# Kernel tuning notes

Measured on AMD Instinct MI355X. Metric: run time of the kernel, lower is better.

## Reference

```python
import jax, jax.numpy as jnp
import numpy as np


def setup_inputs() -> dict:
    bs, L, d, h = 4, 1024, 768, 12
    ne, nm, K, P, F, R = 42, 8, 97, 128, 256, 256
    key = jax.random.key(0)
    ks = jax.random.split(key, 16)
    seq = jax.random.normal(ks[0], (bs, L, d), jnp.float32)
    att = jax.random.uniform(ks[1], (bs, h, L, L), jnp.float32)
    mention_pos = jax.random.randint(ks[2], (bs, ne, nm), 0, 1000)
    n_men = jax.random.randint(ks[3], (bs, ne), 1, nm + 1)
    men_mask = (jnp.arange(nm)[None, None, :] < n_men[..., None]).astype(jnp.float32)
    ht_pairs = jax.random.randint(ks[4], (bs, P, 2), 0, ne)
    s = 0.02
    Wattn = jax.random.normal(ks[5], (d, R)) * s
    battn = jnp.zeros((R,), jnp.float32)
    attn_net = jax.random.normal(ks[6], (K, R)) * s
    Wlin = jax.random.normal(ks[7], (d, 3)) * s
    blin = jnp.zeros((3,), jnp.float32)
    Wseg = jax.random.normal(ks[8], (3, 3, 3, F)) * s  # HWIO conv kernel (SegNet stand-in)
    bseg = jnp.zeros((F,), jnp.float32)
    Whead = jax.random.normal(ks[9], (d + F, d)) * s
    bhead = jnp.zeros((d,), jnp.float32)
    Wtail = jax.random.normal(ks[10], (d + F, d)) * s
    btail = jnp.zeros((d,), jnp.float32)
    lim = (1.0 / (2 * d)) ** 0.5
    bilinear = jax.random.uniform(ks[11], (K, d, d), minval=-lim, maxval=lim)
    bilinear_bias = jax.random.uniform(ks[12], (K,), minval=-lim, maxval=lim)
    return dict(sequence_output=seq, attention=att, men_mask=men_mask,
                mention_pos=mention_pos, ht_pairs=ht_pairs,
                Wattn=Wattn, battn=battn, attn_net=attn_net, Wlin=Wlin, blin=blin,
                Wseg=Wseg, bseg=bseg, Whead=Whead, bhead=bhead, Wtail=Wtail,
                btail=btail, bilinear=bilinear, bilinear_bias=bilinear_bias)


def _forward(sequence_output, attention, men_mask, mention_pos, ht_pairs,
             Wattn, battn, attn_net, Wlin, blin, Wseg, bseg,
             Whead, bhead, Wtail, btail, bilinear, bilinear_bias):
    bs, L, d = sequence_output.shape
    h = attention.shape[1]
    ne, nm = mention_pos.shape[1], mention_pos.shape[2]
    K = attn_net.shape[0]
    OFFSET = 1  # BERT [CLS] offset
    pos = jnp.clip(mention_pos + OFFSET, 0, L - 1)           # [bs,ne,nm]
    b_idx = jnp.arange(bs)[:, None, None]
    # ragged mention gather from sequence_output, zero-padded like the torch loops
    emb = sequence_output[b_idx, pos] * men_mask[..., None]  # [bs,ne,nm,d]
    # per-mention attention rows; attention -> [bs,L,h,L] so we gather on token dim
    A = jnp.transpose(attention, (0, 2, 1, 3))
    m_att = A[b_idx, pos] * men_mask[..., None, None]        # [bs,ne,nm,h,L]
    cnt = jnp.maximum(men_mask.sum(-1), 1.0)                 # mentions per entity
    entity_as = m_att.sum(2) / cnt[..., None, None]          # [bs,ne,h,L] mean over mentions
    # label-wise masked attention pooling over mentions
    neg = (1.0 - men_mask)[..., None] * -1e6                 # [bs,ne,nm,1]
    scores = jnp.tanh(emb @ Wattn + battn) @ attn_net.T + neg  # [bs,ne,nm,K]
    w = jax.nn.softmax(scores, axis=-2)                      # softmax over mentions
    entity_es = jnp.einsum('benk,bend->bekd', w, emb)        # [bs,ne,K,d]
    # context-based channel map (pairwise attention overlap, mean over heads)
    ht = jnp.einsum('bihl,bjhl->bijl', entity_as, entity_as) / h  # [bs,ne,ne,L]
    ht = ht / (ht.sum(-1, keepdims=True) + 1e-5)
    fmap = jnp.einsum('bijl,bld->bijd', ht, sequence_output)      # [bs,ne,ne,d]
    x = fmap @ Wlin + blin                                        # [bs,ne,ne,3]
    seg = jax.lax.conv_general_dilated(x, Wseg, (1, 1), 'SAME',
                                       dimension_numbers=('NHWC', 'HWIO', 'NHWC'))
    attn_map = jax.nn.relu(seg + bseg)                            # [bs,ne,ne,F]
    # pairwise gather (get_hts)
    hi, ti = ht_pairs[..., 0], ht_pairs[..., 1]
    bI = jnp.arange(bs)[:, None]
    F = attn_map.shape[-1]
    htss = attn_map[bI, hi, ti].reshape(-1, F)               # [N,F]
    hss = entity_es[bI, hi].reshape(-1, K, d)                # [N,K,d]
    tss = entity_es[bI, ti].reshape(-1, K, d)
    N = hss.shape[0]
    htr = jnp.broadcast_to(htss[:, None, :], (N, K, F))
    hs = jnp.tanh(jnp.concatenate([hss, htr], -1) @ Whead + bhead)
    ts = jnp.tanh(jnp.concatenate([tss, htr], -1) @ Wtail + btail)
    logits = jnp.einsum('nkd,kdp,nkp->nk', hs, bilinear, ts) + bilinear_bias
    return logits


def reference(sequence_output, attention, men_mask, mention_pos, ht_pairs,
              Wattn, battn, attn_net, Wlin, blin, Wseg, bseg,
              Whead, bhead, Wtail, btail, bilinear, bilinear_bias):
    return _forward(sequence_output, attention, men_mask, mention_pos, ht_pairs,
                    Wattn, battn, attn_net, Wlin, blin, Wseg, bseg,
                    Whead, bhead, Wtail, btail, bilinear, bilinear_bias)
```

## Files before the change

kernel.cpp:

```cpp
#include <hip/hip_runtime.h>
#include <hip/hip_bf16.h>

#define BS 4
#define LL 1024
#define DD 768
#define HH 12
#define NE 42
#define NM 8
#define KK 97
#define PPAIR 128
#define FF 256
#define RR 256
#define NPAIR (BS*PPAIR)
#define MROWS (BS*NE*KK)
#define MT 510
#define NT32 16
#define GRID_BG (8*13*16)

typedef __attribute__((ext_vector_type(8))) short short8;
typedef __attribute__((ext_vector_type(16))) float float16;

__device__ __forceinline__ float fast_tanh(float x){
  x = fminf(fmaxf(x, -15.f), 15.f);
  float e = __expf(2.f*x);
  return 1.f - 2.f/(e + 1.f);
}
__device__ __forceinline__ unsigned short f2bf(float f){
  unsigned int u = __float_as_uint(f);
  unsigned int r = (u + 0x7FFF + ((u>>16)&1)) >> 16;
  return (unsigned short)r;
}
__device__ __forceinline__ float bf2f(unsigned short u){
  return __uint_as_float(((unsigned int)u)<<16);
}
__device__ __forceinline__ void stage16(const void* g, void* l){
  __builtin_amdgcn_global_load_lds(
      (const __attribute__((address_space(1))) void*)g,
      (__attribute__((address_space(3))) void*)l, 16, 0, 0);
}

__global__ void k_emb(const float* __restrict__ seq, const int* __restrict__ mpos,
                      const float* __restrict__ mask, float* __restrict__ emb){
  int idx = blockIdx.x;
  int t = threadIdx.x;
  int b = idx / (NE*NM);
  float mk = mask[idx];
  int pos = mpos[idx] + 1;
  pos = min(max(pos, 0), LL-1);
  const float* src = seq + ((size_t)b*LL + pos)*DD;
  float* dst = emb + (size_t)idx*DD;
  for (int dd = t; dd < DD; dd += 256) dst[dd] = mk * src[dd];
}

__global__ void k_entity_as(const float* __restrict__ att, const int* __restrict__ mpos,
                            const float* __restrict__ mask, float* __restrict__ eas){
  int idx = blockIdx.x;
  int hh = idx % HH; int be = idx / HH;
  int b = be / NE;
  int t = threadIdx.x;
  float cnt = 0.f;
  for (int m=0;m<NM;m++) cnt += mask[be*NM+m];
  float inv = 1.f / fmaxf(cnt, 1.f);
  float acc[4] = {0.f,0.f,0.f,0.f};
  for (int m=0;m<NM;m++){
    float mk = mask[be*NM+m];
    if (mk != 0.f){
      int pos = min(max(mpos[be*NM+m]+1,0), LL-1);
      const float* row = att + (((size_t)b*HH + hh)*LL + pos)*LL;
      acc[0] += mk*row[t]; acc[1] += mk*row[t+256];
      acc[2] += mk*row[t+512]; acc[3] += mk*row[t+768];
    }
  }
  float* dst = eas + (size_t)idx*LL;
  dst[t]=acc[0]*inv; dst[t+256]=acc[1]*inv; dst[t+512]=acc[2]*inv; dst[t+768]=acc[3]*inv;
}

__global__ void k_score1(const float* __restrict__ emb, const float* __restrict__ Wattn,
                         const float* __restrict__ battn, float* __restrict__ tbuf){
  int idx = blockIdx.x; int t = threadIdx.x;
  __shared__ float es[DD];
  es[t]       = emb[(size_t)idx*DD + t];
  es[t+256]   = emb[(size_t)idx*DD + t + 256];
  es[t+512]   = emb[(size_t)idx*DD + t + 512];
  __syncthreads();
  float acc = battn[t];
  for (int dd=0; dd<DD; dd++) acc += es[dd]*Wattn[dd*RR + t];
  tbuf[(size_t)idx*RR + t] = fast_tanh(acc);
}

__global__ void k_scores(const float* __restrict__ tbuf, const float* __restrict__ an,
                         const float* __restrict__ mask, float* __restrict__ w){
  int be = blockIdx.x; int t = threadIdx.x;
  __shared__ float ts_[NM*RR];
  __shared__ float an_s[64*98];
  for (int i=t; i<NM*RR; i+=128) ts_[i] = tbuf[(size_t)be*NM*RR + i];
  float acc[NM];
  #pragma unroll
  for (int m=0;m<NM;m++) acc[m] = 0.f;
  for (int rc=0; rc<RR; rc+=64){
    __syncthreads();
    for (int i=t; i<KK*64; i+=128){
      int kq = i >> 6, r = i & 63;
      an_s[r*98 + kq] = an[kq*RR + rc + r];
    }
    __syncthreads();
    if (t < KK){
      for (int m=0;m<NM;m++){
        float a = 0.f;
        for (int r=0;r<64;r++) a += ts_[m*RR + rc + r]*an_s[r*98 + t];
        acc[m] += a;
      }
    }
  }
  if (t < KK){
    float s[NM];
    #pragma unroll
    for (int m=0;m<NM;m++){
      float mk = mask[be*NM+m];
      s[m] = acc[m] + (1.f - mk)*(-1e6f);
    }
    float mx = s[0];
    #pragma unroll
    for (int m=1;m<NM;m++) mx = fmaxf(mx, s[m]);
    float sum = 0.f; float e[NM];
    #pragma unroll
    for (int m=0;m<NM;m++){ e[m] = __expf(s[m]-mx); sum += e[m]; }
    float invs = 1.f/sum;
    #pragma unroll
    for (int m=0;m<NM;m++) w[((size_t)be*NM+m)*KK + t] = e[m]*invs;
  }
}

__global__ void k_entity_es(const float* __restrict__ emb, const float* __restrict__ w,
                            unsigned short* __restrict__ esf){
  int be = blockIdx.x; int t = threadIdx.x;
  __shared__ float es[NM*DD];
  __shared__ float ws_[NM*KK];
  for (int i = t; i < NM*DD; i += 256) es[i] = emb[(size_t)be*NM*DD + i];
  for (int i = t; i < NM*KK; i += 256) ws_[i] = w[(size_t)be*NM*KK + i];
  __syncthreads();
  for (int idx = t; idx < KK*96; idx += 256){
    int k = idx % KK, d8 = idx / KK;
    int d0 = d8*8;
    float a[8] = {0,0,0,0,0,0,0,0};
    #pragma unroll
    for (int m=0;m<NM;m++){
      float wv = ws_[m*KK + k];
      #pragma unroll
      for (int j=0;j<8;j++) a[j] += wv*es[m*DD + d0 + j];
    }
    int row = be*KK + k;
    int mt = row >> 5, lr = row & 31, ds = d8 >> 1, qq = d8 & 1;
    short8 v;
    #pragma unroll
    for (int j=0;j<8;j++) v[j] = (short)f2bf(a[j]);
    *(short8*)(esf + ((((size_t)mt*48) + ds)*64 + lr + 32*qq)*8) = v;
  }
}

__global__ void k_seqlin(const float* __restrict__ seq, const float* __restrict__ Wlin,
                         float* __restrict__ sl){
  int bl = blockIdx.x; int t = threadIdx.x;
  const float* row = seq + (size_t)bl*DD;
  float a[3] = {0.f,0.f,0.f};
  for (int dd=t; dd<DD; dd+=256){
    float v = row[dd];
    a[0] += v*Wlin[dd*3+0]; a[1] += v*Wlin[dd*3+1]; a[2] += v*Wlin[dd*3+2];
  }
  __shared__ float red[256];
  float res[3];
  for (int c=0;c<3;c++){
    red[t] = a[c]; __syncthreads();
    for (int off=128; off>0; off>>=1){ if (t<off) red[t]+=red[t+off]; __syncthreads(); }
    res[c] = red[0]; __syncthreads();
  }
  if (t==0){ sl[bl*3+0]=res[0]; sl[bl*3+1]=res[1]; sl[bl*3+2]=res[2]; }
}

__global__ void k_ht_x(const float* __restrict__ eas, const float* __restrict__ sl,
                       const float* __restrict__ blin, float* __restrict__ x){
  int idx = blockIdx.x;
  int j = idx % NE; int i = (idx/NE)%NE; int b = idx/(NE*NE);
  int t = threadIdx.x;
  int w = t >> 6, lane = t & 63;
  const float* ai = eas + ((size_t)(b*NE+i))*HH*LL;
  const float* aj = eas + ((size_t)(b*NE+j))*HH*LL;
  float v[4];
  #pragma unroll
  for (int it=0; it<4; it++){
    int l = t + it*256;
    float acc=0.f;
    #pragma unroll
    for (int hh2=0; hh2<HH; hh2++) acc += ai[hh2*LL + l]*aj[hh2*LL + l];
    v[it] = acc * (1.f/HH);
  }
  __shared__ float wsum[4];
  __shared__ float xred[4][3];
  float s = v[0]+v[1]+v[2]+v[3];
  s += __shfl_xor(s, 1);  s += __shfl_xor(s, 2);  s += __shfl_xor(s, 4);
  s += __shfl_xor(s, 8);  s += __shfl_xor(s, 16); s += __shfl_xor(s, 32);
  if (lane == 0) wsum[w] = s;
  __syncthreads();
  float inv = 1.f/((wsum[0]+wsum[1]+wsum[2]+wsum[3]) + 1e-5f);
  float xa[3]={0.f,0.f,0.f};
  #pragma unroll
  for (int it=0; it<4; it++){
    int l = t + it*256;
    float wv = v[it]*inv;
    const float* s3 = sl + ((size_t)b*LL + l)*3;
    xa[0]+=wv*s3[0]; xa[1]+=wv*s3[1]; xa[2]+=wv*s3[2];
  }
  #pragma unroll
  for (int c=0;c<3;c++){
    float q = xa[c];
    q += __shfl_xor(q, 1);  q += __shfl_xor(q, 2);  q += __shfl_xor(q, 4);
    q += __shfl_xor(q, 8);  q += __shfl_xor(q, 16); q += __shfl_xor(q, 32);
    if (lane == 0) xred[w][c] = q;
  }
  __syncthreads();
  if (t < 3) x[(size_t)idx*3 + t] = xred[0][t]+xred[1][t]+xred[2][t]+xred[3][t] + blin[t];
}

__global__ void k_conv_pairs(const float* __restrict__ x, const int* __restrict__ pairs,
                             const float* __restrict__ Wseg, const float* __restrict__ bseg,
                             float* __restrict__ htss){
  int n = blockIdx.x; int t = threadIdx.x;
  int b = n / PPAIR;
  int hi = pairs[n*2+0], ti = pairs[n*2+1];
  __shared__ float xs[27];
  if (t < 27){
    int di = t/9, dj = (t/3)%3, ci = t%3;
    int ii = hi + di - 1, jj = ti + dj - 1;
    float v = 0.f;
    if (ii>=0 && ii<NE && jj>=0 && jj<NE) v = x[(((size_t)b*NE+ii)*NE+jj)*3 + ci];
    xs[t] = v;
  }
  __syncthreads();
  float acc = bseg[t];
  #pragma unroll
  for (int tap=0; tap<27; tap++) acc += xs[tap]*Wseg[tap*FF + t];
  htss[(size_t)n*FF + t] = fmaxf(acc, 0.f);
}

__global__ void k_pair_proj(const float* __restrict__ htss, const float* __restrict__ Wb,
                            const float* __restrict__ bias, float* __restrict__ outp){
  int n = blockIdx.x; int t = threadIdx.x;
  __shared__ float hs_s[FF];
  hs_s[t] = htss[(size_t)n*FF + t];
  __syncthreads();
  float a0 = bias[t], a1 = bias[t+256], a2 = bias[t+512];
  for (int r=0;r<FF;r++){
    float hv = hs_s[r];
    const float* wr = Wb + (size_t)r*DD;
    a0 += hv*wr[t]; a1 += hv*wr[t+256]; a2 += hv*wr[t+512];
  }
  float* dst = outp + (size_t)n*DD;
  dst[t]=a0; dst[t+256]=a1; dst[t+512]=a2;
}

__global__ void k_wshuffle(const float* __restrict__ src, unsigned short* __restrict__ dst){
  int bi = blockIdx.x;
  int mat = bi / 144; int r = bi % 144;
  int ds = r / 3, ntg = r % 3;
  int t = threadIdx.x;
  size_t mo = (size_t)mat*589824;
  __shared__ float ls[16][260];
  #pragma unroll
  for (int i=0;i<16;i++)
    ls[i][t] = src[mo + ((size_t)(ds*16+i))*768 + ntg*256 + t];
  __syncthreads();
  #pragma unroll
  for (int it=0; it<2; it++){
    int idx = it*256 + t;
    int pt_l = idx >> 6, lane = idx & 63;
    int nl = pt_l*32 + (lane & 31);
    int qq = lane >> 5;
    short8 v;
    #pragma unroll
    for (int j=0;j<8;j++) v[j] = (short)f2bf(ls[qq*8 + j][nl]);
    *(short8*)(dst + mo + (((size_t)ds*24 + ntg*8 + pt_l)*64 + lane)*8) = v;
  }
}

__global__ __launch_bounds__(256) void k_gemm_frag2(const unsigned short* __restrict__ Af,
    const unsigned short* __restrict__ Bh, const unsigned short* __restrict__ Bt,
    unsigned short* __restrict__ Ch, unsigned short* __restrict__ Ct){
  int mt = blockIdx.x / 6, ntg = blockIdx.x % 6;
  int t = threadIdx.x; int w = t >> 6; int lane = t & 63;
  int nt = ntg*4 + w;
  float16 acch = (float16)(0.0f), acct = (float16)(0.0f);
  const unsigned short* ap = Af + (((size_t)mt*48)*64 + lane)*8;
  const unsigned short* bph = Bh + (((size_t)nt)*64 + lane)*8;
  const unsigned short* bpt = Bt + (((size_t)nt)*64 + lane)*8;
  #pragma unroll 4
  for (int ds=0; ds<48; ds++){
    short8 a  = *(const short8*)(ap + (size_t)ds*512);
    short8 bh = *(const short8*)(bph + (size_t)ds*24*512);
    short8 bt = *(const short8*)(bpt + (size_t)ds*24*512);
    acch = __builtin_amdgcn_mfma_f32_32x32x16_bf16(a, bh, acch, 0, 0, 0);
    acct = __builtin_amdgcn_mfma_f32_32x32x16_bf16(a, bt, acct, 0, 0, 0);
  }
  int col = nt*32 + (lane & 31);
  int aq = lane >> 5;
  #pragma unroll
  for (int rI=0;rI<16;rI++){
    int row = mt*32 + (rI&3) + 8*(rI>>2) + 4*aq;
    Ch[(size_t)row*768 + col] = f2bf(acch[rI]);
    Ct[(size_t)row*768 + col] = f2bf(acct[rI]);
  }
}

__global__ void k_hsts(const unsigned short* __restrict__ Ehb, const float* __restrict__ ph,
                       const int* __restrict__ pairs, unsigned short* __restrict__ hsF){
  int bi = blockIdx.x; int nt = bi / KK; int k = bi - nt*KK;
  int t = threadIdx.x;
  __shared__ int ehB[32];
  if (t < 32){
    int n = nt*32 + t; int b = n >> 7;
    ehB[t] = ((b*NE + pairs[n*2+0])*KK + k)*DD;
  }
  __syncthreads();
  unsigned short* dst = hsF + (((size_t)nt*KK + k)*48)*512;
  #pragma unroll 2
  for (int c=0; c<12; c++){
    int L = c*256 + t;
    int ds = L >> 6, lane = L & 63;
    int r = lane & 31, q = lane >> 5;
    int n = nt*32 + r;
    int d0 = ds*16 + q*8;
    short8 ev = *(const short8*)(Ehb + ehB[r] + d0);
    float4 p0 = *(const float4*)(ph + (size_t)n*DD + d0);
    float4 p1 = *(const float4*)(ph + (size_t)n*DD + d0 + 4);
    float pf[8] = {p0.x,p0.y,p0.z,p0.w,p1.x,p1.y,p1.z,p1.w};
    short8 v;
    #pragma unroll
    for (int j=0;j<8;j++) v[j] = (short)f2bf(fast_tanh(bf2f((unsigned short)ev[j]) + pf[j]));
    *(short8*)(dst + (size_t)ds*512 + lane*8) = v;
  }
}

__global__ void k_outinit(const float* __restrict__ bias, float* __restrict__ out){
  int i = blockIdx.x*256 + threadIdx.x;
  if (i < NPAIR*KK) out[i] = bias[i % KK];
}

__global__ __launch_bounds__(512,4) void k_bil_gemm(
    const unsigned short* __restrict__ hsF, const unsigned short* __restrict__ Etb,
    const float* __restrict__ pt_, const unsigned short* __restrict__ Bfrag,
    const int* __restrict__ pairs, float* __restrict__ out){
  int xcd = blockIdx.x & 7; int g = blockIdx.x >> 3;
  int ps = g & 3; int nt = (g >> 2) & 3; int kgrp = g >> 4;
  int k = kgrp*8 + xcd;
  if (k >= KK) return;
  int n0 = nt*128;
  int t = threadIdx.x; int w = t >> 6; int lane = t & 63;
  int wr = w >> 1, wc = w & 1;
  __shared__ int etB[128];
  __shared__ unsigned short aS[2][4][512];
  __shared__ unsigned short bS[2][6][512];
  __shared__ float redbuf[4][2][32];
  if (t < 128){
    int n = n0 + t; int b = n >> 7;
    etB[t] = ((b*NE + pairs[n*2+1])*KK + k)*DD;
  }
  __syncthreads();
  int aq = lane >> 5;
  const unsigned short* gp0;
  unsigned short* lp0s[2];
  const unsigned short* gp1 = nullptr;
  unsigned short* lp1s[2] = {nullptr, nullptr};
  size_t gstep0, gstep1 = 0;
  if (w < 4){
    gp0 = hsF + (((size_t)(nt*4 + w)*KK + k)*48)*512 + lane*8;
    gstep0 = 512;
    lp0s[0] = &aS[0][w][0]; lp0s[1] = &aS[1][w][0];
  } else {
    gp0 = Bfrag + ((size_t)k*1152 + (size_t)(ps*6 + (w-4)))*512 + lane*8;
    gstep0 = 24*512;
    lp0s[0] = &bS[0][w-4][0]; lp0s[1] = &bS[1][w-4][0];
  }
  int nch = 1;
  if (w < 2){
    gp1 = Bfrag + ((size_t)k*1152 + (size_t)(ps*6 + 4 + w))*512 + lane*8;
    gstep1 = 24*512;
    lp1s[0] = &bS[0][4+w][0]; lp1s[1] = &bS[1][4+w][0];
    nch = 2;
  }
  float16 acc0 = (float16)(0.f), acc1 = (float16)(0.f), acc2 = (float16)(0.f);
  stage16(gp0, lp0s[0]);
  if (nch == 2) stage16(gp1, lp1s[0]);
  for (int ds=0; ds<48; ds++){
    int buf = ds & 1;
    if (ds < 47){
      stage16(gp0 + (size_t)(ds+1)*gstep0, lp0s[buf^1]);
      if (nch == 2) stage16(gp1 + (size_t)(ds+1)*gstep1, lp1s[buf^1]);
      if (nch == 2) asm volatile("s_waitcnt vmcnt(2)" ::: "memory");
      else          asm volatile("s_waitcnt vmcnt(1)" ::: "memory");
    } else {
      asm volatile("s_waitcnt vmcnt(0)" ::: "memory");
    }
    asm volatile("s_barrier" ::: "memory");
    short8 a  = *(const short8*)&aS[buf][wr][lane*8];
    short8 b0 = *(const short8*)&bS[buf][wc  ][lane*8];
    short8 b1 = *(const short8*)&bS[buf][wc+2][lane*8];
    short8 b2 = *(const short8*)&bS[buf][wc+4][lane*8];
    acc0 = __builtin_amdgcn_mfma_f32_32x32x16_bf16(a, b0, acc0, 0, 0, 0);
    acc1 = __builtin_amdgcn_mfma_f32_32x32x16_bf16(a, b1, acc1, 0, 0, 0);
    acc2 = __builtin_amdgcn_mfma_f32_32x32x16_bf16(a, b2, acc2, 0, 0, 0);
    asm volatile("s_barrier" ::: "memory");
  }
  int pb0 = ps*6 + wc;
  #pragma unroll
  for (int rI=0; rI<16; rI++){
    int row = (rI&3) + 8*(rI>>2) + 4*aq;
    int nloc = wr*32 + row;
    int eb = etB[nloc];
    const float* ptp = pt_ + (size_t)(n0 + nloc)*DD;
    int colb = lane & 31;
    int c0 = (pb0+0)*32 + colb, c1 = (pb0+2)*32 + colb, c2 = (pb0+4)*32 + colb;
    float s = acc0[rI]*fast_tanh(bf2f(Etb[eb + c0]) + ptp[c0])
            + acc1[rI]*fast_tanh(bf2f(Etb[eb + c1]) + ptp[c1])
            + acc2[rI]*fast_tanh(bf2f(Etb[eb + c2]) + ptp[c2]);
    s += __shfl_xor(s, 1);  s += __shfl_xor(s, 2);
    s += __shfl_xor(s, 4);  s += __shfl_xor(s, 8);
    s += __shfl_xor(s, 16);
    if ((lane & 31) == 0) redbuf[wr][wc][row] = s;
  }
  __syncthreads();
  if (t < 128){
    atomicAdd(&out[(size_t)(n0 + t)*KK + k],
              redbuf[t>>5][0][t&31] + redbuf[t>>5][1][t&31]);
  }
}

extern "C" void kernel_launch(void* const* d_in, const int* in_sizes, int n_in,
                              void* d_out, int out_size, void* d_ws, size_t ws_size,
                              hipStream_t stream){
  const float* seq      = (const float*)d_in[0];
  const float* att      = (const float*)d_in[1];
  const float* mask     = (const float*)d_in[2];
  const int*   mpos     = (const int*)d_in[3];
  const int*   pairs    = (const int*)d_in[4];
  const float* Wattn    = (const float*)d_in[5];
  const float* battn    = (const float*)d_in[6];
  const float* attn_net = (const float*)d_in[7];
  const float* Wlin     = (const float*)d_in[8];
  const float* blin     = (const float*)d_in[9];
  const float* Wseg     = (const float*)d_in[10];
  const float* bseg     = (const float*)d_in[11];
  const float* Whead    = (const float*)d_in[12];
  const float* bhead    = (const float*)d_in[13];
  const float* Wtail    = (const float*)d_in[14];
  const float* btail    = (const float*)d_in[15];
  const float* bil      = (const float*)d_in[16];
  const float* bilb     = (const float*)d_in[17];
  float* out = (float*)d_out;

  char* ws = (char*)d_ws;
  size_t off = 0;
  auto allocB = [&](size_t nbytes)->char*{
    char* p = ws + off;
    off += (nbytes + 255) & ~(size_t)255;
    return p;
  };
  unsigned short* BF     = (unsigned short*)allocB((size_t)KK*589824*2);
  unsigned short* Ehb    = (unsigned short*)allocB((size_t)MT*32*768*2);
  unsigned short* Etb    = (unsigned short*)allocB((size_t)MT*32*768*2);
  unsigned short* WheadF = (unsigned short*)allocB((size_t)589824*2);
  unsigned short* WtailF = (unsigned short*)allocB((size_t)589824*2);
  float* phb  = (float*)allocB((size_t)NPAIR*DD*4);
  float* ptb  = (float*)allocB((size_t)NPAIR*DD*4);
  size_t hsF_bytes = (size_t)NT32*KK*48*512*2;
  char* uni = allocB(hsF_bytes);
  size_t uoff = 0;
  auto ualloc = [&](size_t nbytes)->char*{
    char* p = uni + uoff;
    uoff += (nbytes + 255) & ~(size_t)255;
    return p;
  };
  float* emb  = (float*)ualloc((size_t)BS*NE*NM*DD*4);
  float* tbuf = (float*)ualloc((size_t)BS*NE*NM*RR*4);
  float* wsm  = (float*)ualloc((size_t)BS*NE*NM*KK*4);
  float* eas  = (float*)ualloc((size_t)BS*NE*HH*LL*4);
  float* sl   = (float*)ualloc((size_t)BS*LL*3*4);
  float* xb   = (float*)ualloc((size_t)BS*NE*NE*3*4);
  float* htss = (float*)ualloc((size_t)NPAIR*FF*4);
  unsigned short* esf = (unsigned short*)ualloc((size_t)MT*48*64*8*2);
  unsigned short* hsF = (unsigned short*)uni;

  k_outinit<<<(NPAIR*KK+255)/256, 256, 0, stream>>>(bilb, out);
  k_emb<<<BS*NE*NM, 256, 0, stream>>>(seq, mpos, mask, emb);
  k_score1<<<BS*NE*NM, 256, 0, stream>>>(emb, Wattn, battn, tbuf);
  k_scores<<<BS*NE, 128, 0, stream>>>(tbuf, attn_net, mask, wsm);
  k_entity_as<<<BS*NE*HH, 256, 0, stream>>>(att, mpos, mask, eas);
  k_entity_es<<<BS*NE, 256, 0, stream>>>(emb, wsm, esf);
  k_seqlin<<<BS*LL, 256, 0, stream>>>(seq, Wlin, sl);
  k_ht_x<<<BS*NE*NE, 256, 0, stream>>>(eas, sl, blin, xb);
  k_conv_pairs<<<NPAIR, 256, 0, stream>>>(xb, pairs, Wseg, bseg, htss);
  k_pair_proj<<<NPAIR, 256, 0, stream>>>(htss, Whead + 768*768, bhead, phb);
  k_pair_proj<<<NPAIR, 256, 0, stream>>>(htss, Wtail + 768*768, btail, ptb);
  k_wshuffle<<<144, 256, 0, stream>>>(Whead, WheadF);
  k_wshuffle<<<144, 256, 0, stream>>>(Wtail, WtailF);
  k_wshuffle<<<KK*144, 256, 0, stream>>>(bil, BF);
  k_gemm_frag2<<<MT*6, 256, 0, stream>>>(esf, WheadF, WtailF, Ehb, Etb);
  k_hsts<<<NT32*KK, 256, 0, stream>>>(Ehb, phb, pairs, hsF);
  k_bil_gemm<<<GRID_BG, 512, 0, stream>>>(hsF, Etb, ptb, BF, pairs, out);
}
```

Measured before the change: 892.9 us.

## Fuse small kernels and deepen bilinear GEMM K-step with unified LDS staging

Merges the mention embedding gather with the attention score projection, fuses the head and tail pair projections into a single kernel, and replaces the tree reduction in the seq-linear kernel with wavefront shuffles. The bilinear MFMA GEMM now stages two K-slices per iteration into one unified LDS buffer, halving the iteration and barrier count, and its launch-bounds occupancy hint is raised from 4 to 6. These changes aim to cut launch overhead, redundant global reads and synchronisation. The higher occupancy target may squeeze registers, and the larger LDS footprint may limit how many blocks fit per CU.

```diff
diff --git a/kernel.cpp b/kernel.cpp
--- a/kernel.cpp
+++ b/kernel.cpp
@@ -39,8 +39,10 @@
       (__attribute__((address_space(3))) void*)l, 16, 0, 0);
 }
 
-__global__ void k_emb(const float* __restrict__ seq, const int* __restrict__ mpos,
-                      const float* __restrict__ mask, float* __restrict__ emb){
+__global__ void k_emb_score1(const float* __restrict__ seq, const int* __restrict__ mpos,
+                             const float* __restrict__ mask, const float* __restrict__ Wattn,
+                             const float* __restrict__ battn, float* __restrict__ emb,
+                             float* __restrict__ tbuf){
   int idx = blockIdx.x;
   int t = threadIdx.x;
   int b = idx / (NE*NM);
@@ -49,7 +51,14 @@
   pos = min(max(pos, 0), LL-1);
   const float* src = seq + ((size_t)b*LL + pos)*DD;
   float* dst = emb + (size_t)idx*DD;
-  for (int dd = t; dd < DD; dd += 256) dst[dd] = mk * src[dd];
+  __shared__ float es[DD];
+  float v0 = mk*src[t], v1 = mk*src[t+256], v2 = mk*src[t+512];
+  es[t] = v0; es[t+256] = v1; es[t+512] = v2;
+  dst[t] = v0; dst[t+256] = v1; dst[t+512] = v2;
+  __syncthreads();
+  float acc = battn[t];
+  for (int dd=0; dd<DD; dd++) acc += es[dd]*Wattn[dd*RR + t];
+  tbuf[(size_t)idx*RR + t] = fast_tanh(acc);
 }
 
 __global__ void k_entity_as(const float* __restrict__ att, const int* __restrict__ mpos,
@@ -75,19 +84,6 @@
   dst[t]=acc[0]*inv; dst[t+256]=acc[1]*inv; dst[t+512]=acc[2]*inv; dst[t+768]=acc[3]*inv;
 }
 
-__global__ void k_score1(const float* __restrict__ emb, const float* __restrict__ Wattn,
-                         const float* __restrict__ battn, float* __restrict__ tbuf){
-  int idx = blockIdx.x; int t = threadIdx.x;
-  __shared__ float es[DD];
-  es[t]       = emb[(size_t)idx*DD + t];
-  es[t+256]   = emb[(size_t)idx*DD + t + 256];
-  es[t+512]   = emb[(size_t)idx*DD + t + 512];
-  __syncthreads();
-  float acc = battn[t];
-  for (int dd=0; dd<DD; dd++) acc += es[dd]*Wattn[dd*RR + t];
-  tbuf[(size_t)idx*RR + t] = fast_tanh(acc);
-}
-
 __global__ void k_scores(const float* __restrict__ tbuf, const float* __restrict__ an,
                          const float* __restrict__ mask, float* __restrict__ w){
   int be = blockIdx.x; int t = threadIdx.x;
@@ -161,20 +157,21 @@
 __global__ void k_seqlin(const float* __restrict__ seq, const float* __restrict__ Wlin,
                          float* __restrict__ sl){
   int bl = blockIdx.x; int t = threadIdx.x;
+  int w = t >> 6, lane = t & 63;
   const float* row = seq + (size_t)bl*DD;
-  float a[3] = {0.f,0.f,0.f};
+  float a0=0.f, a1=0.f, a2=0.f;
   for (int dd=t; dd<DD; dd+=256){
     float v = row[dd];
-    a[0] += v*Wlin[dd*3+0]; a[1] += v*Wlin[dd*3+1]; a[2] += v*Wlin[dd*3+2];
-  }
-  __shared__ float red[256];
-  float res[3];
-  for (int c=0;c<3;c++){
-    red[t] = a[c]; __syncthreads();
-    for (int off=128; off>0; off>>=1){ if (t<off) red[t]+=red[t+off]; __syncthreads(); }
-    res[c] = red[0]; __syncthreads();
-  }
-  if (t==0){ sl[bl*3+0]=res[0]; sl[bl*3+1]=res[1]; sl[bl*3+2]=res[2]; }
+    a0 += v*Wlin[dd*3+0]; a1 += v*Wlin[dd*3+1]; a2 += v*Wlin[dd*3+2];
+  }
+  #pragma unroll
+  for (int off=1; off<64; off<<=1){
+    a0 += __shfl_xor(a0, off); a1 += __shfl_xor(a1, off); a2 += __shfl_xor(a2, off);
+  }
+  __shared__ float red[4][3];
+  if (lane == 0){ red[w][0]=a0; red[w][1]=a1; red[w][2]=a2; }
+  __syncthreads();
+  if (t < 3) sl[bl*3+t] = red[0][t]+red[1][t]+red[2][t]+red[3][t];
 }
 
 __global__ void k_ht_x(const float* __restrict__ eas, const float* __restrict__ sl,
@@ -242,20 +239,27 @@
   htss[(size_t)n*FF + t] = fmaxf(acc, 0.f);
 }
 
-__global__ void k_pair_proj(const float* __restrict__ htss, const float* __restrict__ Wb,
-                            const float* __restrict__ bias, float* __restrict__ outp){
+__global__ void k_pair_proj2(const float* __restrict__ htss,
+                             const float* __restrict__ Wh, const float* __restrict__ Wt,
+                             const float* __restrict__ bh, const float* __restrict__ bt,
+                             float* __restrict__ oh, float* __restrict__ ot){
   int n = blockIdx.x; int t = threadIdx.x;
   __shared__ float hs_s[FF];
   hs_s[t] = htss[(size_t)n*FF + t];
   __syncthreads();
-  float a0 = bias[t], a1 = bias[t+256], a2 = bias[t+512];
+  float h0 = bh[t], h1 = bh[t+256], h2 = bh[t+512];
+  float t0 = bt[t], t1 = bt[t+256], t2 = bt[t+512];
   for (int r=0;r<FF;r++){
     float hv = hs_s[r];
-    const float* wr = Wb + (size_t)r*DD;
-    a0 += hv*wr[t]; a1 += hv*wr[t+256]; a2 += hv*wr[t+512];
-  }
-  float* dst = outp + (size_t)n*DD;
-  dst[t]=a0; dst[t+256]=a1; dst[t+512]=a2;
+    const float* wh = Wh + (size_t)r*DD;
+    const float* wt = Wt + (size_t)r*DD;
+    h0 += hv*wh[t]; h1 += hv*wh[t+256]; h2 += hv*wh[t+512];
+    t0 += hv*wt[t]; t1 += hv*wt[t+256]; t2 += hv*wt[t+512];
+  }
+  float* dh = oh + (size_t)n*DD;
+  float* dt = ot + (size_t)n*DD;
+  dh[t]=h0; dh[t+256]=h1; dh[t+512]=h2;
+  dt[t]=t0; dt[t+256]=t1; dt[t+512]=t2;
 }
 
 __global__ void k_wshuffle(const float* __restrict__ src, unsigned short* __restrict__ dst){
@@ -344,7 +348,7 @@
   if (i < NPAIR*KK) out[i] = bias[i % KK];
 }
 
-__global__ __launch_bounds__(512,4) void k_bil_gemm(
+__global__ __launch_bounds__(512,6) void k_bil_gemm(
     const unsigned short* __restrict__ hsF, const unsigned short* __restrict__ Etb,
     const float* __restrict__ pt_, const unsigned short* __restrict__ Bfrag,
     const int* __restrict__ pairs, float* __restrict__ out){
@@ -356,8 +360,7 @@
   int t = threadIdx.x; int w = t >> 6; int lane = t & 63;
   int wr = w >> 1, wc = w & 1;
   __shared__ int etB[128];
-  __shared__ unsigned short aS[2][4][512];
-  __shared__ unsigned short bS[2][6][512];
+  __shared__ unsigned short ldsAB[2][20][512];
   __shared__ float redbuf[4][2][32];
   if (t < 128){
     int n = n0 + t; int b = n >> 7;
@@ -365,48 +368,43 @@
   }
   __syncthreads();
   int aq = lane >> 5;
-  const unsigned short* gp0;
-  unsigned short* lp0s[2];
-  const unsigned short* gp1 = nullptr;
-  unsigned short* lp1s[2] = {nullptr, nullptr};
-  size_t gstep0, gstep1 = 0;
-  if (w < 4){
-    gp0 = hsF + (((size_t)(nt*4 + w)*KK + k)*48)*512 + lane*8;
-    gstep0 = 512;
-    lp0s[0] = &aS[0][w][0]; lp0s[1] = &aS[1][w][0];
-  } else {
-    gp0 = Bfrag + ((size_t)k*1152 + (size_t)(ps*6 + (w-4)))*512 + lane*8;
-    gstep0 = 24*512;
-    lp0s[0] = &bS[0][w-4][0]; lp0s[1] = &bS[1][w-4][0];
-  }
-  int nch = 1;
-  if (w < 2){
-    gp1 = Bfrag + ((size_t)k*1152 + (size_t)(ps*6 + 4 + w))*512 + lane*8;
-    gstep1 = 24*512;
-    lp1s[0] = &bS[0][4+w][0]; lp1s[1] = &bS[1][4+w][0];
-    nch = 2;
-  }
+  const unsigned short* g0 = hsF + ((((size_t)(nt*4 + (w&3))*KK + k)*48) + (w>>2))*512 + (size_t)lane*8;
+  int d21 = w/6, p1 = w - d21*6;
+  const unsigned short* g1 = Bfrag + (size_t)k*589824
+                           + ((size_t)(d21*24 + ps*6 + p1))*512 + (size_t)lane*8;
+  const unsigned short* g2 = Bfrag + (size_t)k*589824
+                           + ((size_t)(1*24 + ps*6 + (w+2)))*512 + (size_t)lane*8;
   float16 acc0 = (float16)(0.f), acc1 = (float16)(0.f), acc2 = (float16)(0.f);
-  stage16(gp0, lp0s[0]);
-  if (nch == 2) stage16(gp1, lp1s[0]);
-  for (int ds=0; ds<48; ds++){
-    int buf = ds & 1;
-    if (ds < 47){
-      stage16(gp0 + (size_t)(ds+1)*gstep0, lp0s[buf^1]);
-      if (nch == 2) stage16(gp1 + (size_t)(ds+1)*gstep1, lp1s[buf^1]);
-      if (nch == 2) asm volatile("s_waitcnt vmcnt(2)" ::: "memory");
-      else          asm volatile("s_waitcnt vmcnt(1)" ::: "memory");
+  {
+    stage16(g0, &ldsAB[0][w][0]);
+    stage16(g1, &ldsAB[0][8+w][0]);
+    if (w < 4) stage16(g2, &ldsAB[0][16+w][0]);
+  }
+  for (int it=0; it<24; ++it){
+    int buf = it & 1;
+    if (it < 23){
+      stage16(g0 + (size_t)(it+1)*1024,  &ldsAB[buf^1][w][0]);
+      stage16(g1 + (size_t)(it+1)*24576, &ldsAB[buf^1][8+w][0]);
+      if (w < 4){
+        stage16(g2 + (size_t)(it+1)*24576, &ldsAB[buf^1][16+w][0]);
+        asm volatile("s_waitcnt vmcnt(3)" ::: "memory");
+      } else {
+        asm volatile("s_waitcnt vmcnt(2)" ::: "memory");
+      }
     } else {
       asm volatile("s_waitcnt vmcnt(0)" ::: "memory");
     }
     asm volatile("s_barrier" ::: "memory");
-    short8 a  = *(const short8*)&aS[buf][wr][lane*8];
-    short8 b0 = *(const short8*)&bS[buf][wc  ][lane*8];
-    short8 b1 = *(const short8*)&bS[buf][wc+2][lane*8];
-    short8 b2 = *(const short8*)&bS[buf][wc+4][lane*8];
-    acc0 = __builtin_amdgcn_mfma_f32_32x32x16_bf16(a, b0, acc0, 0, 0, 0);
-    acc1 = __builtin_amdgcn_mfma_f32_32x32x16_bf16(a, b1, acc1, 0, 0, 0);
-    acc2 = __builtin_amdgcn_mfma_f32_32x32x16_bf16(a, b2, acc2, 0, 0, 0);
+    #pragma unroll
+    for (int d2=0; d2<2; ++d2){
+      short8 a  = *(const short8*)&ldsAB[buf][d2*4+wr][lane*8];
+      short8 b0 = *(const short8*)&ldsAB[buf][8+d2*6+wc  ][lane*8];
+      short8 b1 = *(const short8*)&ldsAB[buf][8+d2*6+wc+2][lane*8];
+      short8 b2 = *(const short8*)&ldsAB[buf][8+d2*6+wc+4][lane*8];
+      acc0 = __builtin_amdgcn_mfma_f32_32x32x16_bf16(a, b0, acc0, 0, 0, 0);
+      acc1 = __builtin_amdgcn_mfma_f32_32x32x16_bf16(a, b1, acc1, 0, 0, 0);
+      acc2 = __builtin_amdgcn_mfma_f32_32x32x16_bf16(a, b2, acc2, 0, 0, 0);
+    }
     asm volatile("s_barrier" ::: "memory");
   }
   int pb0 = ps*6 + wc;
@@ -489,16 +487,15 @@
   unsigned short* hsF = (unsigned short*)uni;
 
   k_outinit<<<(NPAIR*KK+255)/256, 256, 0, stream>>>(bilb, out);
-  k_emb<<<BS*NE*NM, 256, 0, stream>>>(seq, mpos, mask, emb);
-  k_score1<<<BS*NE*NM, 256, 0, stream>>>(emb, Wattn, battn, tbuf);
+  k_emb_score1<<<BS*NE*NM, 256, 0, stream>>>(seq, mpos, mask, Wattn, battn, emb, tbuf);
   k_scores<<<BS*NE, 128, 0, stream>>>(tbuf, attn_net, mask, wsm);
   k_entity_as<<<BS*NE*HH, 256, 0, stream>>>(att, mpos, mask, eas);
   k_entity_es<<<BS*NE, 256, 0, stream>>>(emb, wsm, esf);
   k_seqlin<<<BS*LL, 256, 0, stream>>>(seq, Wlin, sl);
   k_ht_x<<<BS*NE*NE, 256, 0, stream>>>(eas, sl, blin, xb);
   k_conv_pairs<<<NPAIR, 256, 0, stream>>>(xb, pairs, Wseg, bseg, htss);
-  k_pair_proj<<<NPAIR, 256, 0, stream>>>(htss, Whead + 768*768, bhead, phb);
-  k_pair_proj<<<NPAIR, 256, 0, stream>>>(htss, Wtail + 768*768, btail, ptb);
+  k_pair_proj2<<<NPAIR, 256, 0, stream>>>(htss, Whead + 768*768, Wtail + 768*768,
+                                          bhead, btail, phb, ptb);
   k_wshuffle<<<144, 256, 0, stream>>>(Whead, WheadF);
   k_wshuffle<<<144, 256, 0, stream>>>(Wtail, WtailF);
   k_wshuffle<<<KK*144, 256, 0, stream>>>(bil, BF);
```

New measurement: 879.3 us. Within noise of the previous version (-1.5%).
